# Kernel optimization log

Measured on AMD Instinct MI355X. Metric: run time of the kernel, lower is better.

Reference implementation:

```python
import jax, jax.numpy as jnp
import numpy as np

# Constants matching init_kwargs
N_HEADS = 8
D_MODEL = 256
PATCH_NUM = 128
D_K = D_MODEL // N_HEADS  # 32
TEMP = 0.5
EPS = 1e-10


def setup_inputs() -> dict:
    key = jax.random.key(0)
    ks = jax.random.split(key, 20)
    s = 0.02
    d, h, n = D_MODEL, N_HEADS, PATCH_NUM
    inp = {
        "x": jax.random.normal(ks[0], (32, n, d), dtype=jnp.float32),
        "gumbel_u": jax.random.uniform(ks[1], (h, n, n, 2), dtype=jnp.float32),
        "memory_w": jax.random.normal(ks[2], (n, h * d), dtype=jnp.float32) * s,
        "fc_out_w": jax.random.normal(ks[3], (2 * d, d), dtype=jnp.float32) * s,
        "fc_out_b": jnp.zeros((d,), jnp.float32),
        "fc_cat_w": jax.random.normal(ks[4], (d, 2), dtype=jnp.float32) * s,
        "fc_cat_b": jnp.zeros((2,), jnp.float32),
        "wq": jax.random.normal(ks[5], (d, d), dtype=jnp.float32) * s,
        "bq": jnp.zeros((d,), jnp.float32),
        "wk": jax.random.normal(ks[6], (d, d), dtype=jnp.float32) * s,
        "bk": jnp.zeros((d,), jnp.float32),
        "wv": jax.random.normal(ks[7], (d, d), dtype=jnp.float32) * s,
        "bv": jnp.zeros((d,), jnp.float32),
        "out_w": jax.random.normal(ks[8], (d, d), dtype=jnp.float32) * s,
        "out_b": jnp.zeros((d,), jnp.float32),
        "mlp_w1": jax.random.normal(ks[9], (d, d), dtype=jnp.float32) * s,
        "mlp_b1": jnp.zeros((d,), jnp.float32),
        "mlp_w2": jax.random.normal(ks[10], (d, d), dtype=jnp.float32) * s,
        "mlp_b2": jnp.zeros((d,), jnp.float32),
    }
    return inp


def _forward(x, memory_w, fc_out_w, fc_out_b, fc_cat_w, fc_cat_b,
             wq, bq, wk, bk, wv, bv, out_w, out_b,
             mlp_w1, mlp_b1, mlp_w2, mlp_b2, gumbel_u):
    H, N, D = N_HEADS, PATCH_NUM, D_MODEL
    B = x.shape[0]

    # ---- SSConnectionLearning on memory feats ----
    # memory: Embedding(N, d_model*n_heads) -> feats [H, N, D]
    feats = memory_w.reshape(N, H, D).transpose(1, 0, 2)
    # rel_rec gathers row index i (receiver), rel_send gathers col index j (sender)
    senders = jnp.broadcast_to(feats[:, None, :, :], (H, N, N, D))   # feats[j]
    receivers = jnp.broadcast_to(feats[:, :, None, :], (H, N, N, D))  # feats[i]
    pair = jnp.concatenate([senders, receivers], axis=-1)  # [H,N,N,2D]
    hdn = jax.nn.relu(jnp.einsum('hijc,cd->hijd', pair, fc_out_w) + fc_out_b)
    logits = jnp.einsum('hijd,dk->hijk', hdn, fc_cat_w) + fc_cat_b  # [H,N,N,2]

    # gumbel-softmax, hard=True, straight-through
    g = -jnp.log(-jnp.log(gumbel_u + EPS) + EPS)
    y_soft = jax.nn.softmax((logits + g) / TEMP, axis=-1)
    y_hard = jax.nn.one_hot(jnp.argmax(y_soft, axis=-1), 2, dtype=y_soft.dtype)
    y = jax.lax.stop_gradient(y_hard - y_soft) + y_soft
    conn = y[..., 1]  # [H,N,N] learned sparse connection mask

    # ---- PatchIntegration (GELU MLP, dropout = identity in eval) ----
    xm = jax.nn.gelu(x @ mlp_w1 + mlp_b1)
    xm = xm @ mlp_w2 + mlp_b2

    # ---- Multihead attention masked by connection matrix ----
    q = (xm @ wq + bq).reshape(B, N, H, D_K).transpose(0, 2, 1, 3)  # [B,H,N,dk]
    k = (xm @ wk + bk).reshape(B, N, H, D_K).transpose(0, 2, 1, 3)
    v = (xm @ wv + bv).reshape(B, N, H, D_K).transpose(0, 2, 1, 3)
    scale = D_K ** -0.5
    scores = jnp.einsum('bhqd,bhkd->bhqk', q, k) * scale
    # additive mask: blocked where conn==0 (large negative keeps softmax finite)
    scores = scores + (conn[None] - 1.0) * 1e9
    attn = jax.nn.softmax(scores, axis=-1)
    out = jnp.einsum('bhqk,bhkd->bhqd', attn, v)
    out = out.transpose(0, 2, 1, 3).reshape(B, N, H * D_K)
    out = out @ out_w + out_b
    return out


def reference(x, gumbel_u, memory_w, fc_out_w, fc_out_b, fc_cat_w, fc_cat_b,
              wq, bq, wk, bk, wv, bv, out_w, out_b,
              mlp_w1, mlp_b1, mlp_w2, mlp_b2):
    return _forward(x, memory_w, fc_out_w, fc_out_b, fc_cat_w, fc_cat_b,
                    wq, bq, wk, bk, wv, bv, out_w, out_b,
                    mlp_w1, mlp_b1, mlp_w2, mlp_b2, gumbel_u)
```

## Files before the change

kernel.cpp:

```cpp
#include <hip/hip_runtime.h>
#include <hip/hip_bf16.h>
#include <math.h>


typedef short short8 __attribute__((ext_vector_type(8)));
typedef float f32x4 __attribute__((ext_vector_type(4)));

union V8 { uint4 u; short8 s; };

__device__ __forceinline__ float gelu_f(float x) {
    float inner = 0.7978845608028654f * (x + 0.044715f * x * x * x);
    return 0.5f * x * (1.0f + tanhf(inner));
}

__device__ __forceinline__ void split_bf16(float x, ushort& h, ushort& l) {
    __hip_bfloat16 bh = __float2bfloat16(x);
    float hf = __bfloat162float(bh);
    __hip_bfloat16 bl = __float2bfloat16(x - hf);
    h = __builtin_bit_cast(ushort, bh);
    l = __builtin_bit_cast(ushort, bl);
}

__device__ __forceinline__ ushort bf16bits(float x) {
    return __builtin_bit_cast(ushort, __float2bfloat16(x));
}
__device__ __forceinline__ float bits_to_f(ushort v) {
    return __builtin_bit_cast(float, ((uint)v) << 16);
}
__device__ __forceinline__ uint pk(float a, float b) {
    return (uint)bf16bits(a) | ((uint)bf16bits(b) << 16);
}
__device__ __forceinline__ short8 lds_frag(const ushort* p) {
    V8 v; v.u = *(const uint4*)p; return v.s;
}

__global__ __launch_bounds__(256) void k_wprep(
    const float* __restrict__ w0, const float* __restrict__ w1,
    const float* __restrict__ w2, const float* __restrict__ w3,
    const float* __restrict__ w4, const float* __restrict__ w5,
    const float* __restrict__ w6, const float* __restrict__ w7,
    ushort* __restrict__ hi, ushort* __restrict__ lo) {
    int bx = blockIdx.x;
    int m = bx >> 4, ks = (bx >> 1) & 7, nh = bx & 1;
    const float* W = m == 0 ? w0 : m == 1 ? w1 : m == 2 ? w2 : m == 3 ? w3 :
                     m == 4 ? w4 : m == 5 ? w5 : m == 6 ? w6 : w7;
    ushort* Hm = hi + m * 65536;
    ushort* Lm = lo + m * 65536;
    __shared__ __align__(16) float xs[32 * 132];
    int t = threadIdx.x;
    #pragma unroll
    for (int p = 0; p < 4; ++p) {
        int idx = p * 256 + t;
        int row = idx >> 5, c4 = (idx & 31) * 4;
        *(float4*)(xs + row * 132 + c4) =
            *(const float4*)(W + (ks * 32 + row) * 256 + nh * 128 + c4);
    }
    __syncthreads();
    int lane = t & 63, lr = lane & 15, quad = lane >> 4;
    #pragma unroll
    for (int it = 0; it < 2; ++it) {
        int tgl = (t >> 6) + 4 * it;
        int tg = nh * 8 + tgl;
        int nl = tgl * 16 + lr;
        ushort hb[8], lb[8];
        #pragma unroll
        for (int j = 0; j < 8; ++j)
            split_bf16(xs[(quad * 8 + j) * 132 + nl], hb[j], lb[j]);
        uint4 ph = { (uint)hb[0] | ((uint)hb[1] << 16), (uint)hb[2] | ((uint)hb[3] << 16),
                     (uint)hb[4] | ((uint)hb[5] << 16), (uint)hb[6] | ((uint)hb[7] << 16) };
        uint4 pl = { (uint)lb[0] | ((uint)lb[1] << 16), (uint)lb[2] | ((uint)lb[3] << 16),
                     (uint)lb[4] | ((uint)lb[5] << 16), (uint)lb[6] | ((uint)lb[7] << 16) };
        int idx = ((tg * 8 + ks) * 64 + lane) * 8;
        *(uint4*)(Hm + idx) = ph;
        *(uint4*)(Lm + idx) = pl;
    }
}

__global__ __launch_bounds__(256) void k_featproj(
    const float* __restrict__ memory_w,
    const ushort* __restrict__ Whi, const ushort* __restrict__ Wlo,
    float* __restrict__ A, float* __restrict__ Bm) {
    __shared__ __align__(16) ushort xhi[16 * 264], xlo[16 * 264];
    int t = threadIdx.x;
    int rt = blockIdx.x;
    int msel = blockIdx.y & 1, cq = blockIdx.y >> 1;
    #pragma unroll
    for (int ii = 0; ii < 4; ++ii) {
        int f4 = ii * 256 + t;
        int rr = f4 >> 6, c = (f4 & 63) * 4;
        int r = rt * 16 + rr;
        int h = r >> 7, n = r & 127;
        float4 xv = *(const float4*)(memory_w + n * 2048 + h * 256 + c);
        ushort hh[4], ll[4];
        split_bf16(xv.x, hh[0], ll[0]); split_bf16(xv.y, hh[1], ll[1]);
        split_bf16(xv.z, hh[2], ll[2]); split_bf16(xv.w, hh[3], ll[3]);
        uint2 ph = { (uint)hh[0] | ((uint)hh[1] << 16), (uint)hh[2] | ((uint)hh[3] << 16) };
        uint2 pl = { (uint)ll[0] | ((uint)ll[1] << 16), (uint)ll[2] | ((uint)ll[3] << 16) };
        *(uint2*)(xhi + rr * 264 + c) = ph;
        *(uint2*)(xlo + rr * 264 + c) = pl;
    }
    __syncthreads();
    int l = t & 63, w = t >> 6;
    int lr = l & 15, quad = l >> 4;
    int tg = cq * 4 + w;
    const uint4* H4 = (const uint4*)(Whi + (6 + msel) * 65536);
    const uint4* L4 = (const uint4*)(Wlo + (6 + msel) * 65536);
    const ushort* ah = xhi + lr * 264 + quad * 8;
    const ushort* al = xlo + lr * 264 + quad * 8;
    f32x4 acc = {};
    #pragma unroll 4
    for (int ks = 0; ks < 8; ++ks) {
        short8 a_h = lds_frag(ah + ks * 32);
        short8 a_l = lds_frag(al + ks * 32);
        int off = (tg * 8 + ks) * 64 + l;
        V8 bh, bl; bh.u = H4[off]; bl.u = L4[off];
        acc = __builtin_amdgcn_mfma_f32_16x16x32_bf16(a_h, bh.s, acc, 0, 0, 0);
        acc = __builtin_amdgcn_mfma_f32_16x16x32_bf16(a_l, bh.s, acc, 0, 0, 0);
        acc = __builtin_amdgcn_mfma_f32_16x16x32_bf16(a_h, bl.s, acc, 0, 0, 0);
    }
    float* O = msel ? Bm : A;
    int n0 = tg * 16 + lr;
    #pragma unroll
    for (int r = 0; r < 4; ++r)
        O[(rt * 16 + quad * 4 + r) * 256 + n0] = acc[r];
}

__global__ __launch_bounds__(256) void k_conn(
    const float* __restrict__ A, const float* __restrict__ Bm,
    const float* __restrict__ fc_out_b, const float* __restrict__ fc_cat_w,
    const float* __restrict__ fc_cat_b, const float* __restrict__ gumbel_u,
    ushort* __restrict__ maskb) {
    int bx = blockIdx.x;
    int h = bx >> 6, it = (bx >> 3) & 7, jt = bx & 7;
    int i0 = it * 16, j0 = jt * 16;
    int t = threadIdx.x;
    int il = t >> 4, jl = t & 15;
    __shared__ __align__(16) float sA[16 * 260], sB[16 * 260];
    #pragma unroll
    for (int p = 0; p < 4; ++p) {
        int idx = p * 256 + t;
        int rr = idx >> 6, c = (idx & 63) * 4;
        *(float4*)(sA + rr * 260 + c) =
            *(const float4*)(A + (h * 128 + j0 + rr) * 256 + c);
        float4 bv = *(const float4*)(Bm + (h * 128 + i0 + rr) * 256 + c);
        float4 fb = *(const float4*)(fc_out_b + c);
        bv.x += fb.x; bv.y += fb.y; bv.z += fb.z; bv.w += fb.w;
        *(float4*)(sB + rr * 260 + c) = bv;
    }
    __syncthreads();
    const float* Ar = sA + jl * 260;
    const float* Br = sB + il * 260;
    float l0 = fc_cat_b[0], l1 = fc_cat_b[1];
    #pragma unroll 4
    for (int d4 = 0; d4 < 64; ++d4) {
        int d = d4 * 4;
        float4 av = *(const float4*)(Ar + d);
        float4 bv = *(const float4*)(Br + d);
        float4 cwA = *(const float4*)(fc_cat_w + d * 2);
        float4 cwB = *(const float4*)(fc_cat_w + d * 2 + 4);
        float h0 = fmaxf(av.x + bv.x, 0.f);
        float h1 = fmaxf(av.y + bv.y, 0.f);
        float h2 = fmaxf(av.z + bv.z, 0.f);
        float h3 = fmaxf(av.w + bv.w, 0.f);
        l0 += h0 * cwA.x + h1 * cwA.z + h2 * cwB.x + h3 * cwB.z;
        l1 += h0 * cwA.y + h1 * cwA.w + h2 * cwB.y + h3 * cwB.w;
    }
    int i = i0 + il, j = j0 + jl;
    float2 uu = *(const float2*)(gumbel_u + ((h * 128 + i) * 128 + j) * 2);
    float g0 = -logf(-logf(uu.x + 1e-10f) + 1e-10f);
    float g1 = -logf(-logf(uu.y + 1e-10f) + 1e-10f);
    bool on = (l1 + g1) > (l0 + g0);
    maskb[(h * 128 + i) * 128 + j] = bf16bits(on ? 0.f : -1e9f);
}

template <int ACT>
__global__ __launch_bounds__(256) void k_gemm16(
    const float* __restrict__ X, const ushort* __restrict__ Whi,
    const ushort* __restrict__ Wlo, const float* __restrict__ bias,
    float* __restrict__ Y) {
    __shared__ __align__(16) ushort xhi[16 * 264], xlo[16 * 264];
    int t = threadIdx.x;
    int r0 = blockIdx.x * 16;
    #pragma unroll
    for (int ii = 0; ii < 4; ++ii) {
        int f4 = ii * 256 + t;
        int row = f4 >> 6, c = (f4 & 63) * 4;
        float4 xv = *(const float4*)(X + (r0 + row) * 256 + c);
        ushort h[4], l[4];
        split_bf16(xv.x, h[0], l[0]); split_bf16(xv.y, h[1], l[1]);
        split_bf16(xv.z, h[2], l[2]); split_bf16(xv.w, h[3], l[3]);
        uint2 ph = { (uint)h[0] | ((uint)h[1] << 16), (uint)h[2] | ((uint)h[3] << 16) };
        uint2 pl = { (uint)l[0] | ((uint)l[1] << 16), (uint)l[2] | ((uint)l[3] << 16) };
        *(uint2*)(xhi + row * 264 + c) = ph;
        *(uint2*)(xlo + row * 264 + c) = pl;
    }
    __syncthreads();
    int l = t & 63, w = t >> 6;
    int lr = l & 15, quad = l >> 4;
    int tg = blockIdx.y * 4 + w;
    const ushort* ah = xhi + lr * 264 + quad * 8;
    const ushort* al = xlo + lr * 264 + quad * 8;
    const uint4* H4 = (const uint4*)Whi;
    const uint4* L4 = (const uint4*)Wlo;
    f32x4 acc = {};
    #pragma unroll 4
    for (int ks = 0; ks < 8; ++ks) {
        short8 a_h = lds_frag(ah + ks * 32);
        short8 a_l = lds_frag(al + ks * 32);
        int off = (tg * 8 + ks) * 64 + l;
        V8 bh, bl; bh.u = H4[off]; bl.u = L4[off];
        acc = __builtin_amdgcn_mfma_f32_16x16x32_bf16(a_h, bh.s, acc, 0, 0, 0);
        acc = __builtin_amdgcn_mfma_f32_16x16x32_bf16(a_l, bh.s, acc, 0, 0, 0);
        acc = __builtin_amdgcn_mfma_f32_16x16x32_bf16(a_h, bl.s, acc, 0, 0, 0);
    }
    int n0 = tg * 16 + lr;
    float bs = bias[n0];
    #pragma unroll
    for (int r = 0; r < 4; ++r) {
        float o = acc[r] + bs;
        if (ACT) o = gelu_f(o);
        Y[(r0 + quad * 4 + r) * 256 + n0] = o;
    }
}

__global__ __launch_bounds__(256) void k_qkv(
    const float* __restrict__ X, const ushort* __restrict__ Whi,
    const ushort* __restrict__ Wlo,
    const float* __restrict__ Bq, const float* __restrict__ Bk,
    const float* __restrict__ Bv,
    float* __restrict__ Q, float* __restrict__ K, float* __restrict__ V) {
    __shared__ __align__(16) ushort xhi[16 * 264], xlo[16 * 264];
    int t = threadIdx.x;
    int r0 = blockIdx.x * 16;
    int osel = blockIdx.y >> 2, cq = blockIdx.y & 3;
    #pragma unroll
    for (int ii = 0; ii < 4; ++ii) {
        int f4 = ii * 256 + t;
        int row = f4 >> 6, c = (f4 & 63) * 4;
        float4 xv = *(const float4*)(X + (r0 + row) * 256 + c);
        ushort h[4], l[4];
        split_bf16(xv.x, h[0], l[0]); split_bf16(xv.y, h[1], l[1]);
        split_bf16(xv.z, h[2], l[2]); split_bf16(xv.w, h[3], l[3]);
        uint2 ph = { (uint)h[0] | ((uint)h[1] << 16), (uint)h[2] | ((uint)h[3] << 16) };
        uint2 pl = { (uint)l[0] | ((uint)l[1] << 16), (uint)l[2] | ((uint)l[3] << 16) };
        *(uint2*)(xhi + row * 264 + c) = ph;
        *(uint2*)(xlo + row * 264 + c) = pl;
    }
    __syncthreads();
    int l = t & 63, w = t >> 6;
    int lr = l & 15, quad = l >> 4;
    int tg = cq * 4 + w;
    const ushort* ah = xhi + lr * 264 + quad * 8;
    const ushort* al = xlo + lr * 264 + quad * 8;
    const uint4* H4 = (const uint4*)(Whi + (2 + osel) * 65536);
    const uint4* L4 = (const uint4*)(Wlo + (2 + osel) * 65536);
    f32x4 acc = {};
    #pragma unroll 4
    for (int ks = 0; ks < 8; ++ks) {
        short8 a_h = lds_frag(ah + ks * 32);
        short8 a_l = lds_frag(al + ks * 32);
        int off = (tg * 8 + ks) * 64 + l;
        V8 bh, bl; bh.u = H4[off]; bl.u = L4[off];
        acc = __builtin_amdgcn_mfma_f32_16x16x32_bf16(a_h, bh.s, acc, 0, 0, 0);
        acc = __builtin_amdgcn_mfma_f32_16x16x32_bf16(a_l, bh.s, acc, 0, 0, 0);
        acc = __builtin_amdgcn_mfma_f32_16x16x32_bf16(a_h, bl.s, acc, 0, 0, 0);
    }
    const float* Bp = osel == 0 ? Bq : osel == 1 ? Bk : Bv;
    float* O = osel == 0 ? Q : osel == 1 ? K : V;
    int n0 = tg * 16 + lr;
    float bs = Bp[n0];
    #pragma unroll
    for (int r = 0; r < 4; ++r)
        O[(r0 + quad * 4 + r) * 256 + n0] = acc[r] + bs;
}

__global__ __launch_bounds__(256) void k_attn_mfma(
    const float* __restrict__ Q, const float* __restrict__ K,
    const float* __restrict__ V, const ushort* __restrict__ maskb,
    float* __restrict__ AO) {
    int bx = blockIdx.x;
    int b = bx >> 4, h = (bx >> 1) & 7, rh = bx & 1;
    int t = threadIdx.x;
    int lane = t & 63, w = t >> 6;
    __shared__ __align__(16) ushort vT[32 * 136];
    __shared__ __align__(16) ushort ps[64 * 136];
    #pragma unroll
    for (int it = 0; it < 4; ++it) {
        int f4 = it * 256 + t;
        int key = f4 >> 3, dq = (f4 & 7) * 4;
        float4 vv = *(const float4*)(V + b * 32768 + key * 256 + h * 32 + dq);
        vT[(dq + 0) * 136 + key] = bf16bits(vv.x);
        vT[(dq + 1) * 136 + key] = bf16bits(vv.y);
        vT[(dq + 2) * 136 + key] = bf16bits(vv.z);
        vT[(dq + 3) * 136 + key] = bf16bits(vv.w);
    }
    __syncthreads();
    int lr = lane & 15, quad = lane >> 4;
    int rt = rh * 4 + w;
    const float* qp = Q + b * 32768 + (rt * 16 + lr) * 256 + h * 32 + quad * 8;
    float4 q0 = *(const float4*)qp, q1 = *(const float4*)(qp + 4);
    V8 af;
    af.u.x = pk(q0.x, q0.y); af.u.y = pk(q0.z, q0.w);
    af.u.z = pk(q1.x, q1.y); af.u.w = pk(q1.z, q1.w);
    f32x4 s[8];
    #pragma unroll
    for (int ct = 0; ct < 8; ++ct) {
        const float* kp = K + b * 32768 + (ct * 16 + lr) * 256 + h * 32 + quad * 8;
        float4 k0 = *(const float4*)kp, k1 = *(const float4*)(kp + 4);
        V8 bf_;
        bf_.u.x = pk(k0.x, k0.y); bf_.u.y = pk(k0.z, k0.w);
        bf_.u.z = pk(k1.x, k1.y); bf_.u.w = pk(k1.z, k1.w);
        f32x4 z = {0.f, 0.f, 0.f, 0.f};
        s[ct] = __builtin_amdgcn_mfma_f32_16x16x32_bf16(af.s, bf_.s, z, 0, 0, 0);
    }
    const float scale = 0.17677669529663687f;
    const ushort* mrow = maskb + h * 16384;
    #pragma unroll
    for (int r = 0; r < 4; ++r) {
        int lrow = w * 16 + quad * 4 + r;
        int grow = rt * 16 + quad * 4 + r;
        float sv[8];
        float mx = -3.0e38f;
        #pragma unroll
        for (int ct = 0; ct < 8; ++ct) {
            float bias = bits_to_f(mrow[grow * 128 + ct * 16 + lr]);
            sv[ct] = s[ct][r] * scale + bias;
            mx = fmaxf(mx, sv[ct]);
        }
        mx = fmaxf(mx, __shfl_xor(mx, 1));
        mx = fmaxf(mx, __shfl_xor(mx, 2));
        mx = fmaxf(mx, __shfl_xor(mx, 4));
        mx = fmaxf(mx, __shfl_xor(mx, 8));
        float sum = 0.f;
        #pragma unroll
        for (int ct = 0; ct < 8; ++ct) {
            sv[ct] = __expf(sv[ct] - mx);
            sum += sv[ct];
        }
        sum += __shfl_xor(sum, 1);
        sum += __shfl_xor(sum, 2);
        sum += __shfl_xor(sum, 4);
        sum += __shfl_xor(sum, 8);
        float iv = 1.f / sum;
        #pragma unroll
        for (int ct = 0; ct < 8; ++ct)
            ps[lrow * 136 + ct * 16 + lr] = bf16bits(sv[ct] * iv);
    }
    f32x4 o0 = {}, o1 = {};
    #pragma unroll
    for (int kk = 0; kk < 4; ++kk) {
        short8 pa = lds_frag(ps + (w * 16 + lr) * 136 + kk * 32 + quad * 8);
        short8 v0 = lds_frag(vT + lr * 136 + kk * 32 + quad * 8);
        short8 v1 = lds_frag(vT + (16 + lr) * 136 + kk * 32 + quad * 8);
        o0 = __builtin_amdgcn_mfma_f32_16x16x32_bf16(pa, v0, o0, 0, 0, 0);
        o1 = __builtin_amdgcn_mfma_f32_16x16x32_bf16(pa, v1, o1, 0, 0, 0);
    }
    #pragma unroll
    for (int r = 0; r < 4; ++r) {
        int grow = rt * 16 + quad * 4 + r;
        float* op = AO + b * 32768 + grow * 256 + h * 32;
        op[lr] = o0[r];
        op[16 + lr] = o1[r];
    }
}

extern "C" void kernel_launch(void* const* d_in, const int* in_sizes, int n_in,
                              void* d_out, int out_size, void* d_ws, size_t ws_size,
                              hipStream_t stream) {
    const float* x        = (const float*)d_in[0];
    const float* gumbel_u = (const float*)d_in[1];
    const float* memory_w = (const float*)d_in[2];
    const float* fc_out_w = (const float*)d_in[3];
    const float* fc_out_b = (const float*)d_in[4];
    const float* fc_cat_w = (const float*)d_in[5];
    const float* fc_cat_b = (const float*)d_in[6];
    const float* wq       = (const float*)d_in[7];
    const float* bq       = (const float*)d_in[8];
    const float* wk       = (const float*)d_in[9];
    const float* bk       = (const float*)d_in[10];
    const float* wv_      = (const float*)d_in[11];
    const float* bv_      = (const float*)d_in[12];
    const float* out_w    = (const float*)d_in[13];
    const float* out_b    = (const float*)d_in[14];
    const float* mlp_w1   = (const float*)d_in[15];
    const float* mlp_b1   = (const float*)d_in[16];
    const float* mlp_w2   = (const float*)d_in[17];
    const float* mlp_b2   = (const float*)d_in[18];

    float* ws    = (float*)d_ws;
    float* A     = ws;
    float* Bm    = ws + 262144;
    ushort* mask = (ushort*)(ws + 524288);
    float* hbuf  = ws + 589824;
    float* xm    = ws + 1638400;
    float* q     = ws + 2686976;
    float* k     = ws + 3735552;
    float* v     = ws + 4784128;
    float* ao    = ws + 5832704;
    ushort* wf_hi = (ushort*)(ws + 6881280);
    ushort* wf_lo = wf_hi + 8 * 65536;
    float* out   = (float*)d_out;

    k_wprep<<<dim3(128), dim3(256), 0, stream>>>(
        mlp_w1, mlp_w2, wq, wk, wv_, out_w, fc_out_w, fc_out_w + 65536,
        wf_hi, wf_lo);
    k_featproj<<<dim3(64, 8), dim3(256), 0, stream>>>(memory_w, wf_hi, wf_lo, A, Bm);
    k_conn<<<dim3(512), dim3(256), 0, stream>>>(A, Bm, fc_out_b, fc_cat_w, fc_cat_b,
                                                gumbel_u, mask);
    k_gemm16<1><<<dim3(256, 4), dim3(256), 0, stream>>>(x, wf_hi + 0 * 65536,
                                                        wf_lo + 0 * 65536, mlp_b1, hbuf);
    k_gemm16<0><<<dim3(256, 4), dim3(256), 0, stream>>>(hbuf, wf_hi + 1 * 65536,
                                                        wf_lo + 1 * 65536, mlp_b2, xm);
    k_qkv<<<dim3(256, 12), dim3(256), 0, stream>>>(xm, wf_hi, wf_lo, bq, bk, bv_, q, k, v);
    k_attn_mfma<<<dim3(512), dim3(256), 0, stream>>>(q, k, v, mask, ao);
    k_gemm16<0><<<dim3(256, 4), dim3(256), 0, stream>>>(ao, wf_hi + 5 * 65536,
                                                        wf_lo + 5 * 65536, out_b, out);
}
```

Before: 161.4 us.

## Fuse MLP and QKV projections into one kernel emitting bf16 Q/K/V

Merges the two MLP GEMMs and the Q/K/V projection into a single 512-thread kernel. Each block keeps its 16-row activation tile in LDS as hi/lo bf16 across all three stages, so the hbuf and xm intermediates no longer go through global memory and three launches become one. Q/K/V are now written as bf16, which halves attention input traffic and removes in-kernel packing, at a small precision cost. The trade-off is only 256 blocks, each doing serial work across the stages, so parallelism drops compared with the former 1024–3072 block grids.

```diff
diff --git a/kernel.cpp b/kernel.cpp
--- a/kernel.cpp
+++ b/kernel.cpp
@@ -12,7 +12,6 @@
     float inner = 0.7978845608028654f * (x + 0.044715f * x * x * x);
     return 0.5f * x * (1.0f + tanhf(inner));
 }
-
 __device__ __forceinline__ void split_bf16(float x, ushort& h, ushort& l) {
     __hip_bfloat16 bh = __float2bfloat16(x);
     float hf = __bfloat162float(bh);
@@ -20,15 +19,11 @@
     h = __builtin_bit_cast(ushort, bh);
     l = __builtin_bit_cast(ushort, bl);
 }
-
 __device__ __forceinline__ ushort bf16bits(float x) {
     return __builtin_bit_cast(ushort, __float2bfloat16(x));
 }
 __device__ __forceinline__ float bits_to_f(ushort v) {
     return __builtin_bit_cast(float, ((uint)v) << 16);
-}
-__device__ __forceinline__ uint pk(float a, float b) {
-    return (uint)bf16bits(a) | ((uint)bf16bits(b) << 16);
 }
 __device__ __forceinline__ short8 lds_frag(const ushort* p) {
     V8 v; v.u = *(const uint4*)p; return v.s;
@@ -108,7 +103,7 @@
     const ushort* ah = xhi + lr * 264 + quad * 8;
     const ushort* al = xlo + lr * 264 + quad * 8;
     f32x4 acc = {};
-    #pragma unroll 4
+    #pragma unroll
     for (int ks = 0; ks < 8; ++ks) {
         short8 a_h = lds_frag(ah + ks * 32);
         short8 a_l = lds_frag(al + ks * 32);
@@ -173,7 +168,225 @@
     maskb[(h * 128 + i) * 128 + j] = bf16bits(on ? 0.f : -1e9f);
 }
 
-template <int ACT>
+__global__ __launch_bounds__(512) void k_fused3(
+    const float* __restrict__ X,
+    const ushort* __restrict__ Whi, const ushort* __restrict__ Wlo,
+    const float* __restrict__ b1, const float* __restrict__ b2,
+    const float* __restrict__ Bq, const float* __restrict__ Bk,
+    const float* __restrict__ Bv,
+    ushort* __restrict__ Q, ushort* __restrict__ K, ushort* __restrict__ V) {
+    __shared__ __align__(16) ushort aHi[16 * 264], aLo[16 * 264];
+    __shared__ __align__(16) ushort bHi[16 * 264], bLo[16 * 264];
+    int t = threadIdx.x;
+    int r0 = blockIdx.x * 16;
+    #pragma unroll
+    for (int ii = 0; ii < 2; ++ii) {
+        int f4 = ii * 512 + t;
+        int row = f4 >> 6, c = (f4 & 63) * 4;
+        float4 xv = *(const float4*)(X + (r0 + row) * 256 + c);
+        ushort h[4], l[4];
+        split_bf16(xv.x, h[0], l[0]); split_bf16(xv.y, h[1], l[1]);
+        split_bf16(xv.z, h[2], l[2]); split_bf16(xv.w, h[3], l[3]);
+        uint2 ph = { (uint)h[0] | ((uint)h[1] << 16), (uint)h[2] | ((uint)h[3] << 16) };
+        uint2 pl = { (uint)l[0] | ((uint)l[1] << 16), (uint)l[2] | ((uint)l[3] << 16) };
+        *(uint2*)(aHi + row * 264 + c) = ph;
+        *(uint2*)(aLo + row * 264 + c) = pl;
+    }
+    __syncthreads();
+    int lane = t & 63, w = t >> 6;
+    int lr = lane & 15, quad = lane >> 4;
+    int aoff = lr * 264 + quad * 8;
+    {
+        const uint4* H4 = (const uint4*)(Whi + 0 * 65536);
+        const uint4* L4 = (const uint4*)(Wlo + 0 * 65536);
+        f32x4 acc[2] = {};
+        #pragma unroll
+        for (int ks = 0; ks < 8; ++ks) {
+            short8 a_h = lds_frag(aHi + aoff + ks * 32);
+            short8 a_l = lds_frag(aLo + aoff + ks * 32);
+            #pragma unroll
+            for (int ti = 0; ti < 2; ++ti) {
+                int off = ((w * 2 + ti) * 8 + ks) * 64 + lane;
+                V8 bh, bl; bh.u = H4[off]; bl.u = L4[off];
+                acc[ti] = __builtin_amdgcn_mfma_f32_16x16x32_bf16(a_h, bh.s, acc[ti], 0, 0, 0);
+                acc[ti] = __builtin_amdgcn_mfma_f32_16x16x32_bf16(a_l, bh.s, acc[ti], 0, 0, 0);
+                acc[ti] = __builtin_amdgcn_mfma_f32_16x16x32_bf16(a_h, bl.s, acc[ti], 0, 0, 0);
+            }
+        }
+        #pragma unroll
+        for (int ti = 0; ti < 2; ++ti) {
+            int n0 = (w * 2 + ti) * 16 + lr;
+            float bb = b1[n0];
+            #pragma unroll
+            for (int r = 0; r < 4; ++r) {
+                float o = gelu_f(acc[ti][r] + bb);
+                ushort hh, ll; split_bf16(o, hh, ll);
+                int ad = (quad * 4 + r) * 264 + n0;
+                bHi[ad] = hh; bLo[ad] = ll;
+            }
+        }
+    }
+    __syncthreads();
+    {
+        const uint4* H4 = (const uint4*)(Whi + 1 * 65536);
+        const uint4* L4 = (const uint4*)(Wlo + 1 * 65536);
+        f32x4 acc[2] = {};
+        #pragma unroll
+        for (int ks = 0; ks < 8; ++ks) {
+            short8 a_h = lds_frag(bHi + aoff + ks * 32);
+            short8 a_l = lds_frag(bLo + aoff + ks * 32);
+            #pragma unroll
+            for (int ti = 0; ti < 2; ++ti) {
+                int off = ((w * 2 + ti) * 8 + ks) * 64 + lane;
+                V8 bh, bl; bh.u = H4[off]; bl.u = L4[off];
+                acc[ti] = __builtin_amdgcn_mfma_f32_16x16x32_bf16(a_h, bh.s, acc[ti], 0, 0, 0);
+                acc[ti] = __builtin_amdgcn_mfma_f32_16x16x32_bf16(a_l, bh.s, acc[ti], 0, 0, 0);
+                acc[ti] = __builtin_amdgcn_mfma_f32_16x16x32_bf16(a_h, bl.s, acc[ti], 0, 0, 0);
+            }
+        }
+        __syncthreads();
+        #pragma unroll
+        for (int ti = 0; ti < 2; ++ti) {
+            int n0 = (w * 2 + ti) * 16 + lr;
+            float bb = b2[n0];
+            #pragma unroll
+            for (int r = 0; r < 4; ++r) {
+                float o = acc[ti][r] + bb;
+                ushort hh, ll; split_bf16(o, hh, ll);
+                int ad = (quad * 4 + r) * 264 + n0;
+                aHi[ad] = hh; aLo[ad] = ll;
+            }
+        }
+    }
+    __syncthreads();
+    {
+        const uint4* Hq = (const uint4*)(Whi + 2 * 65536);
+        const uint4* Lq = (const uint4*)(Wlo + 2 * 65536);
+        const uint4* Hk = (const uint4*)(Whi + 3 * 65536);
+        const uint4* Lk = (const uint4*)(Wlo + 3 * 65536);
+        const uint4* Hv = (const uint4*)(Whi + 4 * 65536);
+        const uint4* Lv = (const uint4*)(Wlo + 4 * 65536);
+        f32x4 aq[2] = {}, ak[2] = {}, av[2] = {};
+        #pragma unroll 2
+        for (int ks = 0; ks < 8; ++ks) {
+            short8 a_h = lds_frag(aHi + aoff + ks * 32);
+            short8 a_l = lds_frag(aLo + aoff + ks * 32);
+            #pragma unroll
+            for (int ti = 0; ti < 2; ++ti) {
+                int off = ((w * 2 + ti) * 8 + ks) * 64 + lane;
+                V8 qh, ql, kh, kl, vh, vl;
+                qh.u = Hq[off]; ql.u = Lq[off];
+                kh.u = Hk[off]; kl.u = Lk[off];
+                vh.u = Hv[off]; vl.u = Lv[off];
+                aq[ti] = __builtin_amdgcn_mfma_f32_16x16x32_bf16(a_h, qh.s, aq[ti], 0, 0, 0);
+                aq[ti] = __builtin_amdgcn_mfma_f32_16x16x32_bf16(a_l, qh.s, aq[ti], 0, 0, 0);
+                aq[ti] = __builtin_amdgcn_mfma_f32_16x16x32_bf16(a_h, ql.s, aq[ti], 0, 0, 0);
+                ak[ti] = __builtin_amdgcn_mfma_f32_16x16x32_bf16(a_h, kh.s, ak[ti], 0, 0, 0);
+                ak[ti] = __builtin_amdgcn_mfma_f32_16x16x32_bf16(a_l, kh.s, ak[ti], 0, 0, 0);
+                ak[ti] = __builtin_amdgcn_mfma_f32_16x16x32_bf16(a_h, kl.s, ak[ti], 0, 0, 0);
+                av[ti] = __builtin_amdgcn_mfma_f32_16x16x32_bf16(a_h, vh.s, av[ti], 0, 0, 0);
+                av[ti] = __builtin_amdgcn_mfma_f32_16x16x32_bf16(a_l, vh.s, av[ti], 0, 0, 0);
+                av[ti] = __builtin_amdgcn_mfma_f32_16x16x32_bf16(a_h, vl.s, av[ti], 0, 0, 0);
+            }
+        }
+        #pragma unroll
+        for (int ti = 0; ti < 2; ++ti) {
+            int n0 = (w * 2 + ti) * 16 + lr;
+            float bq = Bq[n0], bk = Bk[n0], bv = Bv[n0];
+            #pragma unroll
+            for (int r = 0; r < 4; ++r) {
+                int go = (r0 + quad * 4 + r) * 256 + n0;
+                Q[go] = bf16bits(aq[ti][r] + bq);
+                K[go] = bf16bits(ak[ti][r] + bk);
+                V[go] = bf16bits(av[ti][r] + bv);
+            }
+        }
+    }
+}
+
+__global__ __launch_bounds__(256) void k_attn_mfma(
+    const ushort* __restrict__ Q, const ushort* __restrict__ K,
+    const ushort* __restrict__ V, const ushort* __restrict__ maskb,
+    float* __restrict__ AO) {
+    int bx = blockIdx.x;
+    int b = bx >> 4, h = (bx >> 1) & 7, rh = bx & 1;
+    int t = threadIdx.x;
+    int lane = t & 63, w = t >> 6;
+    __shared__ __align__(16) ushort vT[32 * 136];
+    __shared__ __align__(16) ushort ps[64 * 136];
+    #pragma unroll
+    for (int it = 0; it < 2; ++it) {
+        int idx = it * 256 + t;
+        int key = idx >> 2, dq8 = (idx & 3) * 8;
+        V8 vv; vv.u = *(const uint4*)(V + (b * 128 + key) * 256 + h * 32 + dq8);
+        #pragma unroll
+        for (int m = 0; m < 8; ++m)
+            vT[(dq8 + m) * 136 + key] = (ushort)vv.s[m];
+    }
+    __syncthreads();
+    int lr = lane & 15, quad = lane >> 4;
+    int rt = rh * 4 + w;
+    V8 af;
+    af.u = *(const uint4*)(Q + (b * 128 + rt * 16 + lr) * 256 + h * 32 + quad * 8);
+    f32x4 s[8];
+    #pragma unroll
+    for (int ct = 0; ct < 8; ++ct) {
+        V8 bf_;
+        bf_.u = *(const uint4*)(K + (b * 128 + ct * 16 + lr) * 256 + h * 32 + quad * 8);
+        f32x4 z = {0.f, 0.f, 0.f, 0.f};
+        s[ct] = __builtin_amdgcn_mfma_f32_16x16x32_bf16(af.s, bf_.s, z, 0, 0, 0);
+    }
+    const float scale = 0.17677669529663687f;
+    const ushort* mrow = maskb + h * 16384;
+    #pragma unroll
+    for (int r = 0; r < 4; ++r) {
+        int lrow = w * 16 + quad * 4 + r;
+        int grow = rt * 16 + quad * 4 + r;
+        float sv[8];
+        float mx = -3.0e38f;
+        #pragma unroll
+        for (int ct = 0; ct < 8; ++ct) {
+            float bias = bits_to_f(mrow[grow * 128 + ct * 16 + lr]);
+            sv[ct] = s[ct][r] * scale + bias;
+            mx = fmaxf(mx, sv[ct]);
+        }
+        mx = fmaxf(mx, __shfl_xor(mx, 1));
+        mx = fmaxf(mx, __shfl_xor(mx, 2));
+        mx = fmaxf(mx, __shfl_xor(mx, 4));
+        mx = fmaxf(mx, __shfl_xor(mx, 8));
+        float sum = 0.f;
+        #pragma unroll
+        for (int ct = 0; ct < 8; ++ct) {
+            sv[ct] = __expf(sv[ct] - mx);
+            sum += sv[ct];
+        }
+        sum += __shfl_xor(sum, 1);
+        sum += __shfl_xor(sum, 2);
+        sum += __shfl_xor(sum, 4);
+        sum += __shfl_xor(sum, 8);
+        float iv = 1.f / sum;
+        #pragma unroll
+        for (int ct = 0; ct < 8; ++ct)
+            ps[lrow * 136 + ct * 16 + lr] = bf16bits(sv[ct] * iv);
+    }
+    f32x4 o0 = {}, o1 = {};
+    #pragma unroll
+    for (int kk = 0; kk < 4; ++kk) {
+        short8 pa = lds_frag(ps + (w * 16 + lr) * 136 + kk * 32 + quad * 8);
+        short8 v0 = lds_frag(vT + lr * 136 + kk * 32 + quad * 8);
+        short8 v1 = lds_frag(vT + (16 + lr) * 136 + kk * 32 + quad * 8);
+        o0 = __builtin_amdgcn_mfma_f32_16x16x32_bf16(pa, v0, o0, 0, 0, 0);
+        o1 = __builtin_amdgcn_mfma_f32_16x16x32_bf16(pa, v1, o1, 0, 0, 0);
+    }
+    #pragma unroll
+    for (int r = 0; r < 4; ++r) {
+        int grow = rt * 16 + quad * 4 + r;
+        float* op = AO + b * 32768 + grow * 256 + h * 32;
+        op[lr] = o0[r];
+        op[16 + lr] = o1[r];
+    }
+}
+
 __global__ __launch_bounds__(256) void k_gemm16(
     const float* __restrict__ X, const ushort* __restrict__ Whi,
     const ushort* __restrict__ Wlo, const float* __restrict__ bias,
@@ -203,7 +416,7 @@
     const uint4* H4 = (const uint4*)Whi;
     const uint4* L4 = (const uint4*)Wlo;
     f32x4 acc = {};
-    #pragma unroll 4
+    #pragma unroll
     for (int ks = 0; ks < 8; ++ks) {
         short8 a_h = lds_frag(ah + ks * 32);
         short8 a_l = lds_frag(al + ks * 32);
@@ -216,152 +429,8 @@
     int n0 = tg * 16 + lr;
     float bs = bias[n0];
     #pragma unroll
-    for (int r = 0; r < 4; ++r) {
-        float o = acc[r] + bs;
-        if (ACT) o = gelu_f(o);
-        Y[(r0 + quad * 4 + r) * 256 + n0] = o;
-    }
-}
-
-__global__ __launch_bounds__(256) void k_qkv(
-    const float* __restrict__ X, const ushort* __restrict__ Whi,
-    const ushort* __restrict__ Wlo,
-    const float* __restrict__ Bq, const float* __restrict__ Bk,
-    const float* __restrict__ Bv,
-    float* __restrict__ Q, float* __restrict__ K, float* __restrict__ V) {
-    __shared__ __align__(16) ushort xhi[16 * 264], xlo[16 * 264];
-    int t = threadIdx.x;
-    int r0 = blockIdx.x * 16;
-    int osel = blockIdx.y >> 2, cq = blockIdx.y & 3;
-    #pragma unroll
-    for (int ii = 0; ii < 4; ++ii) {
-        int f4 = ii * 256 + t;
-        int row = f4 >> 6, c = (f4 & 63) * 4;
-        float4 xv = *(const float4*)(X + (r0 + row) * 256 + c);
-        ushort h[4], l[4];
-        split_bf16(xv.x, h[0], l[0]); split_bf16(xv.y, h[1], l[1]);
-        split_bf16(xv.z, h[2], l[2]); split_bf16(xv.w, h[3], l[3]);
-        uint2 ph = { (uint)h[0] | ((uint)h[1] << 16), (uint)h[2] | ((uint)h[3] << 16) };
-        uint2 pl = { (uint)l[0] | ((uint)l[1] << 16), (uint)l[2] | ((uint)l[3] << 16) };
-        *(uint2*)(xhi + row * 264 + c) = ph;
-        *(uint2*)(xlo + row * 264 + c) = pl;
-    }
-    __syncthreads();
-    int l = t & 63, w = t >> 6;
-    int lr = l & 15, quad = l >> 4;
-    int tg = cq * 4 + w;
-    const ushort* ah = xhi + lr * 264 + quad * 8;
-    const ushort* al = xlo + lr * 264 + quad * 8;
-    const uint4* H4 = (const uint4*)(Whi + (2 + osel) * 65536);
-    const uint4* L4 = (const uint4*)(Wlo + (2 + osel) * 65536);
-    f32x4 acc = {};
-    #pragma unroll 4
-    for (int ks = 0; ks < 8; ++ks) {
-        short8 a_h = lds_frag(ah + ks * 32);
-        short8 a_l = lds_frag(al + ks * 32);
-        int off = (tg * 8 + ks) * 64 + l;
-        V8 bh, bl; bh.u = H4[off]; bl.u = L4[off];
-        acc = __builtin_amdgcn_mfma_f32_16x16x32_bf16(a_h, bh.s, acc, 0, 0, 0);
-        acc = __builtin_amdgcn_mfma_f32_16x16x32_bf16(a_l, bh.s, acc, 0, 0, 0);
-        acc = __builtin_amdgcn_mfma_f32_16x16x32_bf16(a_h, bl.s, acc, 0, 0, 0);
-    }
-    const float* Bp = osel == 0 ? Bq : osel == 1 ? Bk : Bv;
-    float* O = osel == 0 ? Q : osel == 1 ? K : V;
-    int n0 = tg * 16 + lr;
-    float bs = Bp[n0];
-    #pragma unroll
     for (int r = 0; r < 4; ++r)
-        O[(r0 + quad * 4 + r) * 256 + n0] = acc[r] + bs;
-}
-
-__global__ __launch_bounds__(256) void k_attn_mfma(
-    const float* __restrict__ Q, const float* __restrict__ K,
-    const float* __restrict__ V, const ushort* __restrict__ maskb,
-    float* __restrict__ AO) {
-    int bx = blockIdx.x;
-    int b = bx >> 4, h = (bx >> 1) & 7, rh = bx & 1;
-    int t = threadIdx.x;
-    int lane = t & 63, w = t >> 6;
-    __shared__ __align__(16) ushort vT[32 * 136];
-    __shared__ __align__(16) ushort ps[64 * 136];
-    #pragma unroll
-    for (int it = 0; it < 4; ++it) {
-        int f4 = it * 256 + t;
-        int key = f4 >> 3, dq = (f4 & 7) * 4;
-        float4 vv = *(const float4*)(V + b * 32768 + key * 256 + h * 32 + dq);
-        vT[(dq + 0) * 136 + key] = bf16bits(vv.x);
-        vT[(dq + 1) * 136 + key] = bf16bits(vv.y);
-        vT[(dq + 2) * 136 + key] = bf16bits(vv.z);
-        vT[(dq + 3) * 136 + key] = bf16bits(vv.w);
-    }
-    __syncthreads();
-    int lr = lane & 15, quad = lane >> 4;
-    int rt = rh * 4 + w;
-    const float* qp = Q + b * 32768 + (rt * 16 + lr) * 256 + h * 32 + quad * 8;
-    float4 q0 = *(const float4*)qp, q1 = *(const float4*)(qp + 4);
-    V8 af;
-    af.u.x = pk(q0.x, q0.y); af.u.y = pk(q0.z, q0.w);
-    af.u.z = pk(q1.x, q1.y); af.u.w = pk(q1.z, q1.w);
-    f32x4 s[8];
-    #pragma unroll
-    for (int ct = 0; ct < 8; ++ct) {
-        const float* kp = K + b * 32768 + (ct * 16 + lr) * 256 + h * 32 + quad * 8;
-        float4 k0 = *(const float4*)kp, k1 = *(const float4*)(kp + 4);
-        V8 bf_;
-        bf_.u.x = pk(k0.x, k0.y); bf_.u.y = pk(k0.z, k0.w);
-        bf_.u.z = pk(k1.x, k1.y); bf_.u.w = pk(k1.z, k1.w);
-        f32x4 z = {0.f, 0.f, 0.f, 0.f};
-        s[ct] = __builtin_amdgcn_mfma_f32_16x16x32_bf16(af.s, bf_.s, z, 0, 0, 0);
-    }
-    const float scale = 0.17677669529663687f;
-    const ushort* mrow = maskb + h * 16384;
-    #pragma unroll
-    for (int r = 0; r < 4; ++r) {
-        int lrow = w * 16 + quad * 4 + r;
-        int grow = rt * 16 + quad * 4 + r;
-        float sv[8];
-        float mx = -3.0e38f;
-        #pragma unroll
-        for (int ct = 0; ct < 8; ++ct) {
-            float bias = bits_to_f(mrow[grow * 128 + ct * 16 + lr]);
-            sv[ct] = s[ct][r] * scale + bias;
-            mx = fmaxf(mx, sv[ct]);
-        }
-        mx = fmaxf(mx, __shfl_xor(mx, 1));
-        mx = fmaxf(mx, __shfl_xor(mx, 2));
-        mx = fmaxf(mx, __shfl_xor(mx, 4));
-        mx = fmaxf(mx, __shfl_xor(mx, 8));
-        float sum = 0.f;
-        #pragma unroll
-        for (int ct = 0; ct < 8; ++ct) {
-            sv[ct] = __expf(sv[ct] - mx);
-            sum += sv[ct];
-        }
-        sum += __shfl_xor(sum, 1);
-        sum += __shfl_xor(sum, 2);
-        sum += __shfl_xor(sum, 4);
-        sum += __shfl_xor(sum, 8);
-        float iv = 1.f / sum;
-        #pragma unroll
-        for (int ct = 0; ct < 8; ++ct)
-            ps[lrow * 136 + ct * 16 + lr] = bf16bits(sv[ct] * iv);
-    }
-    f32x4 o0 = {}, o1 = {};
-    #pragma unroll
-    for (int kk = 0; kk < 4; ++kk) {
-        short8 pa = lds_frag(ps + (w * 16 + lr) * 136 + kk * 32 + quad * 8);
-        short8 v0 = lds_frag(vT + lr * 136 + kk * 32 + quad * 8);
-        short8 v1 = lds_frag(vT + (16 + lr) * 136 + kk * 32 + quad * 8);
-        o0 = __builtin_amdgcn_mfma_f32_16x16x32_bf16(pa, v0, o0, 0, 0, 0);
-        o1 = __builtin_amdgcn_mfma_f32_16x16x32_bf16(pa, v1, o1, 0, 0, 0);
-    }
-    #pragma unroll
-    for (int r = 0; r < 4; ++r) {
-        int grow = rt * 16 + quad * 4 + r;
-        float* op = AO + b * 32768 + grow * 256 + h * 32;
-        op[lr] = o0[r];
-        op[16 + lr] = o1[r];
-    }
+        Y[(r0 + quad * 4 + r) * 256 + n0] = acc[r] + bs;
 }
 
 extern "C" void kernel_launch(void* const* d_in, const int* in_sizes, int n_in,
@@ -391,13 +460,11 @@
     float* A     = ws;
     float* Bm    = ws + 262144;
     ushort* mask = (ushort*)(ws + 524288);
-    float* hbuf  = ws + 589824;
-    float* xm    = ws + 1638400;
-    float* q     = ws + 2686976;
-    float* k     = ws + 3735552;
-    float* v     = ws + 4784128;
-    float* ao    = ws + 5832704;
-    ushort* wf_hi = (ushort*)(ws + 6881280);
+    ushort* qb   = (ushort*)(ws + 589824);
+    ushort* kb   = (ushort*)(ws + 1114112);
+    ushort* vb   = (ushort*)(ws + 1638400);
+    float* ao    = ws + 2162688;
+    ushort* wf_hi = (ushort*)(ws + 3211264);
     ushort* wf_lo = wf_hi + 8 * 65536;
     float* out   = (float*)d_out;
 
@@ -405,14 +472,11 @@
         mlp_w1, mlp_w2, wq, wk, wv_, out_w, fc_out_w, fc_out_w + 65536,
         wf_hi, wf_lo);
     k_featproj<<<dim3(64, 8), dim3(256), 0, stream>>>(memory_w, wf_hi, wf_lo, A, Bm);
+    k_fused3<<<dim3(256), dim3(512), 0, stream>>>(x, wf_hi, wf_lo, mlp_b1, mlp_b2,
+                                                  bq, bk, bv_, qb, kb, vb);
     k_conn<<<dim3(512), dim3(256), 0, stream>>>(A, Bm, fc_out_b, fc_cat_w, fc_cat_b,
                                                 gumbel_u, mask);
-    k_gemm16<1><<<dim3(256, 4), dim3(256), 0, stream>>>(x, wf_hi + 0 * 65536,
-                                                        wf_lo + 0 * 65536, mlp_b1, hbuf);
-    k_gemm16<0><<<dim3(256, 4), dim3(256), 0, stream>>>(hbuf, wf_hi + 1 * 65536,
-                                                        wf_lo + 1 * 65536, mlp_b2, xm);
-    k_qkv<<<dim3(256, 12), dim3(256), 0, stream>>>(xm, wf_hi, wf_lo, bq, bk, bv_, q, k, v);
-    k_attn_mfma<<<dim3(512), dim3(256), 0, stream>>>(q, k, v, mask, ao);
-    k_gemm16<0><<<dim3(256, 4), dim3(256), 0, stream>>>(ao, wf_hi + 5 * 65536,
-                                                        wf_lo + 5 * 65536, out_b, out);
-}
+    k_attn_mfma<<<dim3(512), dim3(256), 0, stream>>>(qb, kb, vb, mask, ao);
+    k_gemm16<<<dim3(256, 4), dim3(256), 0, stream>>>(ao, wf_hi + 5 * 65536,
+                                                     wf_lo + 5 * 65536, out_b, out);
+}
```

Result: no change. 159.2 us (-1.4%).
